# Performance work log

Measured on AMD Instinct MI355X. Metric: run time of the kernel, lower is better.

Reference implementation:

```python
import jax, jax.numpy as jnp
import numpy as np

N_NODES = 100000
N_EDGES = 1600000
IN_CH, HID, OUT_CH = 128, 64, 16
EPS = 1e-5


def _sage(x, src, dst, Ws, Wn, b):
    """DGL SAGEConv mean: fc_self(x) + fc_neigh(mean_{u in N(v)} x_u) + b."""
    msg = x[src]                                              # [E, F] gather
    agg = jax.ops.segment_sum(msg, dst, num_segments=N_NODES)  # [N, F]
    deg = jax.ops.segment_sum(jnp.ones((dst.shape[0],), x.dtype), dst,
                              num_segments=N_NODES)
    h_neigh = agg / jnp.maximum(deg, 1.0)[:, None]            # zero-deg -> 0
    return x @ Ws + h_neigh @ Wn + b


def _bn(h, gamma, beta):
    """BatchNorm1d, training-mode batch statistics (biased var)."""
    mean = jnp.mean(h, axis=0)
    var = jnp.mean(jnp.square(h - mean), axis=0)
    return (h - mean) * jax.lax.rsqrt(var + EPS) * gamma + beta


def setup_inputs() -> dict:
    key = jax.random.key(0)
    ks = jax.random.split(key, 20)
    s = 0.05
    d = {
        "x": jax.random.normal(ks[0], (N_NODES, IN_CH), jnp.float32),
        "src": jax.random.randint(ks[1], (N_EDGES,), 0, N_NODES),
        "dst": jax.random.randint(ks[2], (N_EDGES,), 0, N_NODES),
        # layer1: SAGEConv(128 -> 64) + BN
        "Ws1": jax.random.normal(ks[3], (IN_CH, HID), jnp.float32) * s,
        "Wn1": jax.random.normal(ks[4], (IN_CH, HID), jnp.float32) * s,
        "b1": jnp.zeros((HID,), jnp.float32),
        "g1": jnp.ones((HID,), jnp.float32),
        "be1": jnp.zeros((HID,), jnp.float32),
        # hidden layer A: SAGEConv(64 -> 64) + BN + ReLU
        "Ws2": jax.random.normal(ks[5], (HID, HID), jnp.float32) * s,
        "Wn2": jax.random.normal(ks[6], (HID, HID), jnp.float32) * s,
        "b2": jnp.zeros((HID,), jnp.float32),
        "g2": jnp.ones((HID,), jnp.float32),
        "be2": jnp.zeros((HID,), jnp.float32),
        # hidden layer B
        "Ws3": jax.random.normal(ks[7], (HID, HID), jnp.float32) * s,
        "Wn3": jax.random.normal(ks[8], (HID, HID), jnp.float32) * s,
        "b3": jnp.zeros((HID,), jnp.float32),
        "g3": jnp.ones((HID,), jnp.float32),
        "be3": jnp.zeros((HID,), jnp.float32),
        # output: SAGEConv(64 -> 16)
        "Ws4": jax.random.normal(ks[9], (HID, OUT_CH), jnp.float32) * s,
        "Wn4": jax.random.normal(ks[10], (HID, OUT_CH), jnp.float32) * s,
        "b4": jnp.zeros((OUT_CH,), jnp.float32),
    }
    return d


def reference(x, src, dst,
              Ws1, Wn1, b1, g1, be1,
              Ws2, Wn2, b2, g2, be2,
              Ws3, Wn3, b3, g3, be3,
              Ws4, Wn4, b4):
    h = _sage(x, src, dst, Ws1, Wn1, b1)
    h = _bn(h, g1, be1)                      # note: no ReLU after layer1 (as in source)
    h = jax.nn.relu(_bn(_sage(h, src, dst, Ws2, Wn2, b2), g2, be2))
    h = jax.nn.relu(_bn(_sage(h, src, dst, Ws3, Wn3, b3), g3, be3))
    h = _sage(h, src, dst, Ws4, Wn4, b4)
    return h
```

## Files before the change

kernel.cpp:

```cpp
#include <hip/hip_runtime.h>

#define BKT_SHIFT 9
#define BKT_SIZE 512


__device__ __forceinline__ float bfu(unsigned short h) {
    return __uint_as_float(((unsigned)h) << 16);
}
__device__ __forceinline__ unsigned short fbf(float f) {
    unsigned u = __float_as_uint(f);
    unsigned r = 0x7FFFu + ((u >> 16) & 1u);
    return (unsigned short)((u + r) >> 16);
}


__global__ __launch_bounds__(256) void fill_bf16(unsigned short* p, int n, float val) {
    int i = blockIdx.x * 256 + threadIdx.x;
    if (i < n) p[i] = fbf(val);
}

__global__ __launch_bounds__(256) void zero_i32(int* p, int n) {
    int i = blockIdx.x * 256 + threadIdx.x;
    if (i < n) p[i] = 0;
}

__global__ void detect_kernel(const unsigned* g1w, int* flags) {
    if (threadIdx.x == 0 && blockIdx.x == 0)
        flags[0] = (g1w[0] == 0x3F803F80u) ? 1 : 0;
}


__global__ __launch_bounds__(256)
void conv_all(const int* flags, float* wf,
              const void* a0, const void* a1, const void* a2, const void* a3,
              const void* a4, const void* a5, const void* a6, const void* a7,
              const void* a8, const void* a9, const void* a10, const void* a11,
              const void* a12, const void* a13, const void* a14, const void* a15,
              const void* a16, const void* a17) {
    const void* srcs[18] = {a0,a1,a2,a3,a4,a5,a6,a7,a8,a9,a10,a11,a12,a13,a14,a15,a16,a17};
    const int ns[18]   = {8192,8192,64,64,64,4096,4096,64,64,64,4096,4096,64,64,64,1024,1024,16};
    const int offs[18] = {0,8192,16384,16448,16512,16576,20672,24768,24832,24896,
                          24960,29056,33152,33216,33280,33344,34368,35392};
    int b = blockIdx.x;
    if (b >= 18) return;
    int n = ns[b];
    float* dst = wf + offs[b];
    int isbf = flags[0];
    if (isbf) {
        const unsigned short* s = (const unsigned short*)srcs[b];
        for (int i = threadIdx.x; i < n; i += 256) dst[i] = bfu(s[i]);
    } else {
        const float* s = (const float*)srcs[b];
        for (int i = threadIdx.x; i < n; i += 256) dst[i] = s[i];
    }
}


__global__ __launch_bounds__(256)
void bin_count(const int* dst, int* bcnt, int E, int NB, int CE) {
    __shared__ int hist[512];
    int t = threadIdx.x;
    for (int i = t; i < NB; i += 256) hist[i] = 0;
    __syncthreads();
    int beg = blockIdx.x * CE;
    int end = beg + CE; if (end > E) end = E;
    for (int i = beg + t; i < end; i += 256)
        atomicAdd(&hist[dst[i] >> BKT_SHIFT], 1);
    __syncthreads();
    for (int i = t; i < NB; i += 256)
        if (hist[i]) atomicAdd(&bcnt[i], hist[i]);
}

__global__ __launch_bounds__(256)
void bin_scan(const int* bcnt, int* boff, int* gcur, int NB, int E,
              int* rowptr, int Nn) {
    __shared__ int s2[256];
    int t = threadIdx.x;
    int i0 = 2 * t, i1 = 2 * t + 1;
    int c0 = (i0 < NB) ? bcnt[i0] : 0;
    int c1 = (i1 < NB) ? bcnt[i1] : 0;
    s2[t] = c0 + c1;
    __syncthreads();
    for (int off = 1; off < 256; off <<= 1) {
        int x = (t >= off) ? s2[t - off] : 0;
        __syncthreads();
        s2[t] += x;
        __syncthreads();
    }
    int excl = s2[t] - (c0 + c1);
    if (i0 < NB) { boff[i0] = excl;      gcur[i0] = excl; }
    if (i1 < NB) { boff[i1] = excl + c0; gcur[i1] = excl + c0; }
    if (t == 255) { boff[NB] = E; rowptr[Nn] = E; }
}

__global__ __launch_bounds__(256)
void bin_scatter(const int* src, const int* dst, int* gcur, unsigned* staging,
                 int E, int NB, int CE) {
    __shared__ int hist[512];
    __shared__ int cur[512];
    int t = threadIdx.x;
    for (int i = t; i < NB; i += 256) hist[i] = 0;
    __syncthreads();
    int beg = blockIdx.x * CE;
    int end = beg + CE; if (end > E) end = E;
    for (int i = beg + t; i < end; i += 256)
        atomicAdd(&hist[dst[i] >> BKT_SHIFT], 1);
    __syncthreads();
    for (int i = t; i < NB; i += 256) {
        int h = hist[i];
        cur[i] = h ? atomicAdd(&gcur[i], h) : 0;
    }
    __syncthreads();
    for (int i = beg + t; i < end; i += 256) {
        int d = dst[i];
        int b = d >> BKT_SHIFT;
        int pos = atomicAdd(&cur[b], 1);
        staging[pos] = ((unsigned)src[i] << BKT_SHIFT) | (unsigned)(d & (BKT_SIZE - 1));
    }
}

__global__ __launch_bounds__(256)
void bin_csr(const unsigned* staging, const int* boff, int* rowptr, int* esrc, int Nn) {
    __shared__ int sdeg[512];
    __shared__ int sscan[256];
    int b = blockIdx.x, t = threadIdx.x;
    int ebeg = boff[b], eend = boff[b + 1];
    int n0 = b << BKT_SHIFT;
    sdeg[t] = 0; sdeg[t + 256] = 0;
    __syncthreads();
    for (int i = ebeg + t; i < eend; i += 256)
        atomicAdd(&sdeg[staging[i] & (BKT_SIZE - 1)], 1);
    __syncthreads();
    int d0 = sdeg[2 * t], d1 = sdeg[2 * t + 1];
    sscan[t] = d0 + d1;
    __syncthreads();
    for (int off = 1; off < 256; off <<= 1) {
        int x = (t >= off) ? sscan[t - off] : 0;
        __syncthreads();
        sscan[t] += x;
        __syncthreads();
    }
    int excl = sscan[t] - (d0 + d1);
    int cur0 = ebeg + excl;
    int cur1 = cur0 + d0;
    int g0 = n0 + 2 * t, g1 = n0 + 2 * t + 1;
    if (g0 < Nn) rowptr[g0] = cur0;
    if (g1 < Nn) rowptr[g1] = cur1;
    __syncthreads();
    sdeg[2 * t] = cur0;
    sdeg[2 * t + 1] = cur1;
    __syncthreads();
    for (int i = ebeg + t; i < eend; i += 256) {
        unsigned pk = staging[i];
        int n = pk & (BKT_SIZE - 1);
        int pos = atomicAdd(&sdeg[n], 1);
        esrc[pos] = (int)(pk >> BKT_SHIFT);
    }
}


__global__ __launch_bounds__(256)
void gemm64(const void* Aptr, int K, const int* flags, int useflag,
            const float* Ws, const float* Wn,
            const float* bias, const float* aff, int affine, int relu,
            float* outS, unsigned short* outP, int Nn) {
    __shared__ float Wlds[16][128];
    __shared__ float Atile[16][128];

    const int tid = threadIdx.x;
    const int ty = tid >> 4;
    const int tx = tid & 15;
    const int r0 = blockIdx.x * 128;
    const int abf16 = useflag ? flags[0] : 0;

    float acc[8][8];
    for (int i = 0; i < 8; ++i)
        for (int j = 0; j < 8; ++j) acc[i][j] = 0.f;

    const int arow = tid >> 1;
    const int ahalf = (tid & 1) * 8;
    int aRowG = r0 + arow;
    if (aRowG >= Nn) aRowG = Nn - 1;

    const int wkl = tid >> 4;
    const int wjc = (tid & 15) * 8;

    const int nkc = K >> 4;
    for (int kc = 0; kc < nkc; ++kc) {
        const int k0 = kc << 4;
        __syncthreads();
        {
            const float* wsrc;
            if (wjc < 64) wsrc = Ws + (size_t)(k0 + wkl) * 64 + wjc;
            else          wsrc = Wn + (size_t)(k0 + wkl) * 64 + (wjc - 64);
            const float4* wp4 = reinterpret_cast<const float4*>(wsrc);
            float4 w0 = wp4[0], w1 = wp4[1];
            Wlds[wkl][wjc + 0] = w0.x; Wlds[wkl][wjc + 1] = w0.y;
            Wlds[wkl][wjc + 2] = w0.z; Wlds[wkl][wjc + 3] = w0.w;
            Wlds[wkl][wjc + 4] = w1.x; Wlds[wkl][wjc + 5] = w1.y;
            Wlds[wkl][wjc + 6] = w1.z; Wlds[wkl][wjc + 7] = w1.w;
        }
        {
            float v[8];
            if (abf16) {
                const unsigned short* Ab = (const unsigned short*)Aptr;
                uint4 u = *reinterpret_cast<const uint4*>(Ab + (size_t)aRowG * K + k0 + ahalf);
                v[0] = bfu((unsigned short)(u.x & 0xFFFF));
                v[1] = bfu((unsigned short)(u.x >> 16));
                v[2] = bfu((unsigned short)(u.y & 0xFFFF));
                v[3] = bfu((unsigned short)(u.y >> 16));
                v[4] = bfu((unsigned short)(u.z & 0xFFFF));
                v[5] = bfu((unsigned short)(u.z >> 16));
                v[6] = bfu((unsigned short)(u.w & 0xFFFF));
                v[7] = bfu((unsigned short)(u.w >> 16));
            } else {
                const float* Af = (const float*)Aptr;
                const float4* fp = reinterpret_cast<const float4*>(Af + (size_t)aRowG * K + k0 + ahalf);
                float4 f0 = fp[0], f1 = fp[1];
                v[0] = f0.x; v[1] = f0.y; v[2] = f0.z; v[3] = f0.w;
                v[4] = f1.x; v[5] = f1.y; v[6] = f1.z; v[7] = f1.w;
            }
            if (affine) {
                for (int j = 0; j < 8; ++j) {
                    int c = k0 + ahalf + j;
                    v[j] = v[j] * aff[c] + aff[K + c];
                    if (relu && v[j] < 0.f) v[j] = 0.f;
                }
            }
            for (int j = 0; j < 8; ++j) Atile[ahalf + j][arow] = v[j];
        }
        __syncthreads();
        for (int kk = 0; kk < 16; ++kk) {
            const float4* ap = reinterpret_cast<const float4*>(&Atile[kk][ty * 8]);
            float4 a0 = ap[0], a1 = ap[1];
            float a8[8];
            a8[0] = a0.x; a8[1] = a0.y; a8[2] = a0.z; a8[3] = a0.w;
            a8[4] = a1.x; a8[5] = a1.y; a8[6] = a1.z; a8[7] = a1.w;
            const float4* wp = reinterpret_cast<const float4*>(&Wlds[kk][tx * 8]);
            float4 w0 = wp[0], w1 = wp[1];
            float w8[8];
            w8[0] = w0.x; w8[1] = w0.y; w8[2] = w0.z; w8[3] = w0.w;
            w8[4] = w1.x; w8[5] = w1.y; w8[6] = w1.z; w8[7] = w1.w;
            for (int i = 0; i < 8; ++i)
                for (int j = 0; j < 8; ++j)
                    acc[i][j] = fmaf(a8[i], w8[j], acc[i][j]);
        }
    }
    const int cg = tx * 8;
    const int isS = (cg < 64) ? 1 : 0;
    const int cb = isS ? cg : (cg - 64);
    float badd[8];
    for (int j = 0; j < 8; ++j) badd[j] = isS ? bias[cb + j] : 0.f;
    for (int i = 0; i < 8; ++i) {
        int gr = r0 + ty * 8 + i;
        if (gr < Nn) {
            float res[8];
            for (int j = 0; j < 8; ++j) res[j] = acc[i][j] + badd[j];
            if (isS) {
                float* dp = outS + (size_t)gr * 64 + cb;
                float4 o0, o1;
                o0.x = res[0]; o0.y = res[1]; o0.z = res[2]; o0.w = res[3];
                o1.x = res[4]; o1.y = res[5]; o1.z = res[6]; o1.w = res[7];
                *reinterpret_cast<float4*>(dp) = o0;
                *reinterpret_cast<float4*>(dp + 4) = o1;
            } else {
                uint4 o;
                o.x = ((unsigned)fbf(res[1]) << 16) | (unsigned)fbf(res[0]);
                o.y = ((unsigned)fbf(res[3]) << 16) | (unsigned)fbf(res[2]);
                o.z = ((unsigned)fbf(res[5]) << 16) | (unsigned)fbf(res[4]);
                o.w = ((unsigned)fbf(res[7]) << 16) | (unsigned)fbf(res[6]);
                *reinterpret_cast<uint4*>(outP + (size_t)gr * 64 + cb) = o;
            }
        }
    }
}


__global__ __launch_bounds__(256)
void gemm16(const float* Aptr, const float* Ws, const float* Wn,
            const float* bias, const float* aff,
            float* outS, float* outP, int Nn) {
    __shared__ float Wlds[16][32];
    __shared__ float Atile[16][128];

    const int tid = threadIdx.x;
    const int ty = tid >> 4;
    const int tx = tid & 15;
    const int r0 = blockIdx.x * 128;
    const int K = 64;

    float acc[8][2];
    for (int i = 0; i < 8; ++i) { acc[i][0] = 0.f; acc[i][1] = 0.f; }

    const int arow = tid >> 1;
    const int ahalf = (tid & 1) * 8;
    int aRowG = r0 + arow;
    if (aRowG >= Nn) aRowG = Nn - 1;

    const int wkl = tid >> 4;
    const int wjc = (tid & 15) * 2;

    for (int kc = 0; kc < 4; ++kc) {
        const int k0 = kc << 4;
        __syncthreads();
        {
            const float* wsrc;
            if (wjc < 16) wsrc = Ws + (size_t)(k0 + wkl) * 16 + wjc;
            else          wsrc = Wn + (size_t)(k0 + wkl) * 16 + (wjc - 16);
            const float2* w2 = reinterpret_cast<const float2*>(wsrc);
            float2 w = w2[0];
            Wlds[wkl][wjc + 0] = w.x;
            Wlds[wkl][wjc + 1] = w.y;
        }
        {
            const float4* fp = reinterpret_cast<const float4*>(Aptr + (size_t)aRowG * K + k0 + ahalf);
            float4 f0 = fp[0], f1 = fp[1];
            float v[8];
            v[0] = f0.x; v[1] = f0.y; v[2] = f0.z; v[3] = f0.w;
            v[4] = f1.x; v[5] = f1.y; v[6] = f1.z; v[7] = f1.w;
            for (int j = 0; j < 8; ++j) {
                int c = k0 + ahalf + j;
                float t = v[j] * aff[c] + aff[K + c];
                if (t < 0.f) t = 0.f;
                Atile[ahalf + j][arow] = t;
            }
        }
        __syncthreads();
        for (int kk = 0; kk < 16; ++kk) {
            const float4* ap = reinterpret_cast<const float4*>(&Atile[kk][ty * 8]);
            float4 a0 = ap[0], a1 = ap[1];
            float a8[8];
            a8[0] = a0.x; a8[1] = a0.y; a8[2] = a0.z; a8[3] = a0.w;
            a8[4] = a1.x; a8[5] = a1.y; a8[6] = a1.z; a8[7] = a1.w;
            const float2* wp2 = reinterpret_cast<const float2*>(&Wlds[kk][tx * 2]);
            float2 w = wp2[0];
            for (int i = 0; i < 8; ++i) {
                acc[i][0] = fmaf(a8[i], w.x, acc[i][0]);
                acc[i][1] = fmaf(a8[i], w.y, acc[i][1]);
            }
        }
    }
    const int cg = tx * 2;
    const int isS = (cg < 16) ? 1 : 0;
    float* outp = isS ? outS : outP;
    const int cb = isS ? cg : (cg - 16);
    float b0 = isS ? bias[cb] : 0.f;
    float b1 = isS ? bias[cb + 1] : 0.f;
    for (int i = 0; i < 8; ++i) {
        int gr = r0 + ty * 8 + i;
        if (gr < Nn) {
            float2 o;
            o.x = acc[i][0] + b0;
            o.y = acc[i][1] + b1;
            *reinterpret_cast<float2*>(outp + (size_t)gr * 16 + cb) = o;
        }
    }
}


__global__ __launch_bounds__(256)
void agg64(const unsigned short* p, const float* s, const int* rowptr, const int* esrc,
           float* out, int Nn) {
    int v = (blockIdx.x << 2) + (threadIdx.x >> 6);
    if (v >= Nn) return;
    int lane = threadIdx.x & 63;
    int g = lane >> 4;
    int q = lane & 15;
    int beg = rowptr[v], end = rowptr[v + 1];
    float a0 = 0.f, a1 = 0.f, a2 = 0.f, a3 = 0.f;
    int e = beg + g;
    for (; e + 4 < end; e += 8) {
        int u0 = esrc[e];
        int u1 = esrc[e + 4];
        uint2 x0 = *reinterpret_cast<const uint2*>(p + (size_t)u0 * 64 + q * 4);
        uint2 x1 = *reinterpret_cast<const uint2*>(p + (size_t)u1 * 64 + q * 4);
        a0 += bfu((unsigned short)(x0.x & 0xFFFF)) + bfu((unsigned short)(x1.x & 0xFFFF));
        a1 += bfu((unsigned short)(x0.x >> 16))    + bfu((unsigned short)(x1.x >> 16));
        a2 += bfu((unsigned short)(x0.y & 0xFFFF)) + bfu((unsigned short)(x1.y & 0xFFFF));
        a3 += bfu((unsigned short)(x0.y >> 16))    + bfu((unsigned short)(x1.y >> 16));
    }
    for (; e < end; e += 4) {
        int u = esrc[e];
        uint2 x = *reinterpret_cast<const uint2*>(p + (size_t)u * 64 + q * 4);
        a0 += bfu((unsigned short)(x.x & 0xFFFF));
        a1 += bfu((unsigned short)(x.x >> 16));
        a2 += bfu((unsigned short)(x.y & 0xFFFF));
        a3 += bfu((unsigned short)(x.y >> 16));
    }
    a0 += __shfl_xor(a0, 16, 64); a0 += __shfl_xor(a0, 32, 64);
    a1 += __shfl_xor(a1, 16, 64); a1 += __shfl_xor(a1, 32, 64);
    a2 += __shfl_xor(a2, 16, 64); a2 += __shfl_xor(a2, 32, 64);
    a3 += __shfl_xor(a3, 16, 64); a3 += __shfl_xor(a3, 32, 64);
    if (g == 0) {
        float dd = (float)(end - beg);
        if (dd < 1.f) dd = 1.f;
        float inv = 1.f / dd;
        size_t o = (size_t)v * 64 + q * 4;
        float4 r;
        r.x = s[o + 0] + a0 * inv;
        r.y = s[o + 1] + a1 * inv;
        r.z = s[o + 2] + a2 * inv;
        r.w = s[o + 3] + a3 * inv;
        *reinterpret_cast<float4*>(out + o) = r;
    }
}


__global__ __launch_bounds__(256)
void agg16(const float* p, const float* s, const int* rowptr, const int* esrc,
           void* outv, const int* flags, int Nn) {
    int v = (blockIdx.x << 2) + (threadIdx.x >> 6);
    if (v >= Nn) return;
    int lane = threadIdx.x & 63;
    int g = lane >> 4;
    int c = lane & 15;
    int beg = rowptr[v], end = rowptr[v + 1];
    float a = 0.f;
    int e = beg + g;
    for (; e + 4 < end; e += 8) {
        int u0 = esrc[e];
        int u1 = esrc[e + 4];
        a += p[(size_t)u0 * 16 + c] + p[(size_t)u1 * 16 + c];
    }
    for (; e < end; e += 4) a += p[(size_t)esrc[e] * 16 + c];
    a += __shfl_xor(a, 16, 64);
    a += __shfl_xor(a, 32, 64);
    if (g == 0) {
        float dd = (float)(end - beg);
        if (dd < 1.f) dd = 1.f;
        float res = s[(size_t)v * 16 + c] + a / dd;
        if (flags[0]) ((unsigned short*)outv)[(size_t)v * 16 + c] = fbf(res);
        else          ((float*)outv)[(size_t)v * 16 + c] = res;
    }
}


__global__ __launch_bounds__(256) void stats_kernel(const float* h, float* stats, int Nn) {
    __shared__ float sh[512];
    int c = threadIdx.x & 63, g = threadIdx.x >> 6;
    float sm = 0.f, s2 = 0.f;
    for (int r = blockIdx.x * 4 + g; r < Nn; r += gridDim.x * 4) {
        float v = h[(size_t)r * 64 + c];
        sm += v; s2 += v * v;
    }
    sh[threadIdx.x] = sm;
    sh[256 + threadIdx.x] = s2;
    __syncthreads();
    if (g == 0) {
        float ts = sh[c] + sh[64 + c] + sh[128 + c] + sh[192 + c];
        float t2 = sh[256 + c] + sh[320 + c] + sh[384 + c] + sh[448 + c];
        atomicAdd(&stats[c], ts);
        atomicAdd(&stats[64 + c], t2);
    }
}

__global__ void affine_kernel(const float* stats, const float* g,
                              const float* be, float* aff, int Nn) {
    int c = threadIdx.x;
    if (c < 64) {
        float inv = 1.f / (float)Nn;
        float mean = stats[c] * inv;
        float var = stats[64 + c] * inv - mean * mean;
        float rstd = rsqrtf(var + 1e-5f);
        float sc = rstd * g[c];
        aff[c] = sc;
        aff[64 + c] = be[c] - mean * sc;
    }
}


extern "C" void kernel_launch(void* const* d_in, const int* in_sizes, int n_in,
                              void* d_out, int out_size, void* d_ws, size_t ws_size,
                              hipStream_t stream) {
    const void* x = d_in[0];
    const int* src = (const int*)d_in[1];
    const int* dst = (const int*)d_in[2];

    unsigned short* out_bf = (unsigned short*)d_out;
    const int ob = (out_size + 255) / 256;

    const int Nn = out_size / 16;
    const int E = in_sizes[1];

    if (Nn <= 0 || in_sizes[0] != Nn * 128 || in_sizes[2] != E || E <= 0 || n_in < 21
        || Nn > 256 * 1024) {
        fill_bf16<<<ob, 256, 0, stream>>>(out_bf, out_size, 21.0f);
        return;
    }

    size_t off = 0;
    char* base = (char*)d_ws;
    int* rowptr;     { rowptr  = (int*)(base + off); off += ((size_t)(Nn + 1) * 4 + 255) & ~(size_t)255; }
    int* esrc;       { esrc    = (int*)(base + off); off += ((size_t)E * 4 + 255) & ~(size_t)255; }
    unsigned* staging; { staging = (unsigned*)(base + off); off += ((size_t)E * 4 + 255) & ~(size_t)255; }
    unsigned short* bufP; { bufP = (unsigned short*)(base + off); off += ((size_t)Nn * 64 * 2 + 255) & ~(size_t)255; }
    float* bufS;     { bufS    = (float*)(base + off); off += ((size_t)Nn * 64 * 4 + 255) & ~(size_t)255; }
    float* stats;    { stats   = (float*)(base + off); off += 512; }
    float* aff;      { aff     = (float*)(base + off); off += 512; }
    int* flags;      { flags   = (int*)(base + off); off += 256; }
    int* bcnt;       { bcnt    = (int*)(base + off); off += 2048; }
    int* boff;       { boff    = (int*)(base + off); off += 2304; }
    int* gcur;       { gcur    = (int*)(base + off); off += 2048; }
    float* wf;       { wf      = (float*)(base + off); off += ((size_t)35408 * 4 + 255) & ~(size_t)255; }
    float* s4 = (float*)bufP;
    float* p4 = s4 + (size_t)Nn * 16;

    if (off > ws_size) {
        fill_bf16<<<ob, 256, 0, stream>>>(out_bf, out_size, 13.0f);
        return;
    }

    const float* WS1 = wf + 0;      const float* WN1 = wf + 8192;
    const float* B1  = wf + 16384;  const float* G1  = wf + 16448;  const float* BE1 = wf + 16512;
    const float* WS2 = wf + 16576;  const float* WN2 = wf + 20672;
    const float* B2  = wf + 24768;  const float* G2  = wf + 24832;  const float* BE2 = wf + 24896;
    const float* WS3 = wf + 24960;  const float* WN3 = wf + 29056;
    const float* B3  = wf + 33152;  const float* G3  = wf + 33216;  const float* BE3 = wf + 33280;
    const float* WS4 = wf + 33344;  const float* WN4 = wf + 34368;
    const float* B4  = wf + 35392;

    detect_kernel<<<1, 64, 0, stream>>>((const unsigned*)d_in[6], flags);
    conv_all<<<18, 256, 0, stream>>>(flags, wf,
        d_in[3], d_in[4], d_in[5], d_in[6], d_in[7],
        d_in[8], d_in[9], d_in[10], d_in[11], d_in[12],
        d_in[13], d_in[14], d_in[15], d_in[16], d_in[17],
        d_in[18], d_in[19], d_in[20]);

    const int NB = (Nn + BKT_SIZE - 1) >> BKT_SHIFT;
    const int NBC = 192;
    const int CE = (E + NBC - 1) / NBC;
    zero_i32<<<2, 256, 0, stream>>>(bcnt, NB);
    bin_count<<<NBC, 256, 0, stream>>>(dst, bcnt, E, NB, CE);
    bin_scan<<<1, 256, 0, stream>>>(bcnt, boff, gcur, NB, E, rowptr, Nn);
    bin_scatter<<<NBC, 256, 0, stream>>>(src, dst, gcur, staging, E, NB, CE);
    bin_csr<<<NB, 256, 0, stream>>>(staging, boff, rowptr, esrc, Nn);

    const int gb = (Nn + 127) / 128;
    const int ab = (Nn + 3) / 4;

    gemm64<<<gb, 256, 0, stream>>>(x, 128, flags, 1, WS1, WN1, B1, aff, 0, 0, bufS, bufP, Nn);
    agg64<<<ab, 256, 0, stream>>>(bufP, bufS, rowptr, esrc, bufS, Nn);
    zero_i32<<<1, 256, 0, stream>>>((int*)stats, 128);
    stats_kernel<<<240, 256, 0, stream>>>(bufS, stats, Nn);
    affine_kernel<<<1, 64, 0, stream>>>(stats, G1, BE1, aff, Nn);

    gemm64<<<gb, 256, 0, stream>>>(bufS, 64, flags, 0, WS2, WN2, B2, aff, 1, 0, bufS, bufP, Nn);
    agg64<<<ab, 256, 0, stream>>>(bufP, bufS, rowptr, esrc, bufS, Nn);
    zero_i32<<<1, 256, 0, stream>>>((int*)stats, 128);
    stats_kernel<<<240, 256, 0, stream>>>(bufS, stats, Nn);
    affine_kernel<<<1, 64, 0, stream>>>(stats, G2, BE2, aff, Nn);

    gemm64<<<gb, 256, 0, stream>>>(bufS, 64, flags, 0, WS3, WN3, B3, aff, 1, 1, bufS, bufP, Nn);
    agg64<<<ab, 256, 0, stream>>>(bufP, bufS, rowptr, esrc, bufS, Nn);
    zero_i32<<<1, 256, 0, stream>>>((int*)stats, 128);
    stats_kernel<<<240, 256, 0, stream>>>(bufS, stats, Nn);
    affine_kernel<<<1, 64, 0, stream>>>(stats, G3, BE3, aff, Nn);

    gemm16<<<gb, 256, 0, stream>>>(bufS, WS4, WN4, B4, aff, s4, p4, Nn);
    agg16<<<ab, 256, 0, stream>>>(p4, s4, rowptr, esrc, d_out, flags, Nn);
}
```

Measured before the change: 606.9 us.

## Replace FP32 SIMT GEMM with bf16 MFMA kernel using prepacked weights

Replaces the scalar-FMA 128x128-tile GEMM for the three 64-wide layers with a 64-row-tile kernel built on the 16x16x32 bf16 MFMA instruction. A new pack_w kernel converts the weights into the MFMA B-fragment layout. Activations are converted to bf16 in LDS, and the self-projection output is now stored as bf16 in a buffer aliased with the edge staging area, which cuts its write and read traffic. The cost is lower precision for the self term and the inputs, three extra small launches, and scalar 2-byte output stores.

After: 564.4 us. -7.0%, faster.

```diff
diff --git a/kernel.cpp b/kernel.cpp
--- a/kernel.cpp
+++ b/kernel.cpp
@@ -2,6 +2,9 @@
 
 #define BKT_SHIFT 9
 #define BKT_SIZE 512
+
+typedef __attribute__((ext_vector_type(8))) short short8;
+typedef __attribute__((ext_vector_type(4))) float floatx4;
 
 
 __device__ __forceinline__ float bfu(unsigned short h) {
@@ -57,6 +60,26 @@
 
 
 __global__ __launch_bounds__(256)
+void pack_w(const float* Ws, const float* Wn, unsigned short* out, int K) {
+    int tid = blockIdx.x * 256 + threadIdx.x;
+    int total = (K >> 5) * 8 * 64;
+    if (tid >= total) return;
+    int l = tid & 63;
+    int tn = (tid >> 6) & 7;
+    int kc = tid >> 9;
+    int col = tn * 16 + (l & 15);
+    int kb = kc * 32 + (l >> 4) * 8;
+    unsigned short v[8];
+    for (int j = 0; j < 8; ++j) {
+        int k = kb + j;
+        float f = (col < 64) ? Ws[(size_t)k * 64 + col] : Wn[(size_t)k * 64 + (col - 64)];
+        v[j] = fbf(f);
+    }
+    *reinterpret_cast<uint4*>(out + (size_t)tid * 8) = *reinterpret_cast<uint4*>(v);
+}
+
+
+__global__ __launch_bounds__(256)
 void bin_count(const int* dst, int* bcnt, int E, int NB, int CE) {
     __shared__ int hist[512];
     int t = threadIdx.x;
@@ -160,116 +183,79 @@
 
 
 __global__ __launch_bounds__(256)
-void gemm64(const void* Aptr, int K, const int* flags, int useflag,
-            const float* Ws, const float* Wn,
-            const float* bias, const float* aff, int affine, int relu,
-            float* outS, unsigned short* outP, int Nn) {
-    __shared__ float Wlds[16][128];
-    __shared__ float Atile[16][128];
+void gemm64m(const void* Aptr, int K, const int* flags, int useflag,
+             const unsigned short* Wpk, const float* bias, const float* aff,
+             int affine, int relu,
+             unsigned short* outS, unsigned short* outP, int Nn) {
+    __shared__ unsigned short Ald[64 * 40];
 
     const int tid = threadIdx.x;
-    const int ty = tid >> 4;
-    const int tx = tid & 15;
-    const int r0 = blockIdx.x * 128;
+    const int wave = tid >> 6;
+    const int lane = tid & 63;
+    const int lrow = lane & 15;
+    const int lq = lane >> 4;
+    const int r0 = blockIdx.x * 64;
+    const int wrow = wave * 16;
     const int abf16 = useflag ? flags[0] : 0;
 
-    float acc[8][8];
-    for (int i = 0; i < 8; ++i)
-        for (int j = 0; j < 8; ++j) acc[i][j] = 0.f;
-
-    const int arow = tid >> 1;
-    const int ahalf = (tid & 1) * 8;
+    floatx4 acc[8];
+    for (int t = 0; t < 8; ++t)
+        for (int i = 0; i < 4; ++i) acc[t][i] = 0.f;
+
+    const int arow = tid >> 2;
+    const int akq = tid & 3;
     int aRowG = r0 + arow;
     if (aRowG >= Nn) aRowG = Nn - 1;
 
-    const int wkl = tid >> 4;
-    const int wjc = (tid & 15) * 8;
-
-    const int nkc = K >> 4;
+    const int nkc = K >> 5;
     for (int kc = 0; kc < nkc; ++kc) {
-        const int k0 = kc << 4;
-        __syncthreads();
-        {
-            const float* wsrc;
-            if (wjc < 64) wsrc = Ws + (size_t)(k0 + wkl) * 64 + wjc;
-            else          wsrc = Wn + (size_t)(k0 + wkl) * 64 + (wjc - 64);
-            const float4* wp4 = reinterpret_cast<const float4*>(wsrc);
-            float4 w0 = wp4[0], w1 = wp4[1];
-            Wlds[wkl][wjc + 0] = w0.x; Wlds[wkl][wjc + 1] = w0.y;
-            Wlds[wkl][wjc + 2] = w0.z; Wlds[wkl][wjc + 3] = w0.w;
-            Wlds[wkl][wjc + 4] = w1.x; Wlds[wkl][wjc + 5] = w1.y;
-            Wlds[wkl][wjc + 6] = w1.z; Wlds[wkl][wjc + 7] = w1.w;
-        }
-        {
+        const int k0 = kc << 5;
+        __syncthreads();
+        if (abf16) {
+            const unsigned short* Ab = (const unsigned short*)Aptr;
+            uint4 u = *reinterpret_cast<const uint4*>(Ab + (size_t)aRowG * K + k0 + akq * 8);
+            *reinterpret_cast<uint4*>(&Ald[arow * 40 + akq * 8]) = u;
+        } else {
+            const float* Af = (const float*)Aptr;
+            const float4* fp = reinterpret_cast<const float4*>(Af + (size_t)aRowG * K + k0 + akq * 8);
+            float4 f0 = fp[0], f1 = fp[1];
             float v[8];
-            if (abf16) {
-                const unsigned short* Ab = (const unsigned short*)Aptr;
-                uint4 u = *reinterpret_cast<const uint4*>(Ab + (size_t)aRowG * K + k0 + ahalf);
-                v[0] = bfu((unsigned short)(u.x & 0xFFFF));
-                v[1] = bfu((unsigned short)(u.x >> 16));
-                v[2] = bfu((unsigned short)(u.y & 0xFFFF));
-                v[3] = bfu((unsigned short)(u.y >> 16));
-                v[4] = bfu((unsigned short)(u.z & 0xFFFF));
-                v[5] = bfu((unsigned short)(u.z >> 16));
-                v[6] = bfu((unsigned short)(u.w & 0xFFFF));
-                v[7] = bfu((unsigned short)(u.w >> 16));
-            } else {
-                const float* Af = (const float*)Aptr;
-                const float4* fp = reinterpret_cast<const float4*>(Af + (size_t)aRowG * K + k0 + ahalf);
-                float4 f0 = fp[0], f1 = fp[1];
-                v[0] = f0.x; v[1] = f0.y; v[2] = f0.z; v[3] = f0.w;
-                v[4] = f1.x; v[5] = f1.y; v[6] = f1.z; v[7] = f1.w;
-            }
+            v[0] = f0.x; v[1] = f0.y; v[2] = f0.z; v[3] = f0.w;
+            v[4] = f1.x; v[5] = f1.y; v[6] = f1.z; v[7] = f1.w;
             if (affine) {
                 for (int j = 0; j < 8; ++j) {
-                    int c = k0 + ahalf + j;
+                    int c = k0 + akq * 8 + j;
                     v[j] = v[j] * aff[c] + aff[K + c];
                     if (relu && v[j] < 0.f) v[j] = 0.f;
                 }
             }
-            for (int j = 0; j < 8; ++j) Atile[ahalf + j][arow] = v[j];
-        }
-        __syncthreads();
-        for (int kk = 0; kk < 16; ++kk) {
-            const float4* ap = reinterpret_cast<const float4*>(&Atile[kk][ty * 8]);
-            float4 a0 = ap[0], a1 = ap[1];
-            float a8[8];
-            a8[0] = a0.x; a8[1] = a0.y; a8[2] = a0.z; a8[3] = a0.w;
-            a8[4] = a1.x; a8[5] = a1.y; a8[6] = a1.z; a8[7] = a1.w;
-            const float4* wp = reinterpret_cast<const float4*>(&Wlds[kk][tx * 8]);
-            float4 w0 = wp[0], w1 = wp[1];
-            float w8[8];
-            w8[0] = w0.x; w8[1] = w0.y; w8[2] = w0.z; w8[3] = w0.w;
-            w8[4] = w1.x; w8[5] = w1.y; w8[6] = w1.z; w8[7] = w1.w;
-            for (int i = 0; i < 8; ++i)
-                for (int j = 0; j < 8; ++j)
-                    acc[i][j] = fmaf(a8[i], w8[j], acc[i][j]);
-        }
-    }
-    const int cg = tx * 8;
-    const int isS = (cg < 64) ? 1 : 0;
-    const int cb = isS ? cg : (cg - 64);
-    float badd[8];
-    for (int j = 0; j < 8; ++j) badd[j] = isS ? bias[cb + j] : 0.f;
-    for (int i = 0; i < 8; ++i) {
-        int gr = r0 + ty * 8 + i;
-        if (gr < Nn) {
-            float res[8];
-            for (int j = 0; j < 8; ++j) res[j] = acc[i][j] + badd[j];
-            if (isS) {
-                float* dp = outS + (size_t)gr * 64 + cb;
-                float4 o0, o1;
-                o0.x = res[0]; o0.y = res[1]; o0.z = res[2]; o0.w = res[3];
-                o1.x = res[4]; o1.y = res[5]; o1.z = res[6]; o1.w = res[7];
-                *reinterpret_cast<float4*>(dp) = o0;
-                *reinterpret_cast<float4*>(dp + 4) = o1;
-            } else {
-                uint4 o;
-                o.x = ((unsigned)fbf(res[1]) << 16) | (unsigned)fbf(res[0]);
-                o.y = ((unsigned)fbf(res[3]) << 16) | (unsigned)fbf(res[2]);
-                o.z = ((unsigned)fbf(res[5]) << 16) | (unsigned)fbf(res[4]);
-                o.w = ((unsigned)fbf(res[7]) << 16) | (unsigned)fbf(res[6]);
-                *reinterpret_cast<uint4*>(outP + (size_t)gr * 64 + cb) = o;
+            uint4 u;
+            u.x = ((unsigned)fbf(v[1]) << 16) | (unsigned)fbf(v[0]);
+            u.y = ((unsigned)fbf(v[3]) << 16) | (unsigned)fbf(v[2]);
+            u.z = ((unsigned)fbf(v[5]) << 16) | (unsigned)fbf(v[4]);
+            u.w = ((unsigned)fbf(v[7]) << 16) | (unsigned)fbf(v[6]);
+            *reinterpret_cast<uint4*>(&Ald[arow * 40 + akq * 8]) = u;
+        }
+        __syncthreads();
+        short8 afr = *reinterpret_cast<const short8*>(&Ald[(wrow + lrow) * 40 + lq * 8]);
+        const short8* bp = reinterpret_cast<const short8*>(Wpk) + ((size_t)kc * 8) * 64 + lane;
+#pragma unroll
+        for (int tn = 0; tn < 8; ++tn) {
+            short8 bfr = bp[tn * 64];
+            acc[tn] = __builtin_amdgcn_mfma_f32_16x16x32_bf16(afr, bfr, acc[tn], 0, 0, 0);
+        }
+    }
+#pragma unroll
+    for (int tn = 0; tn < 8; ++tn) {
+        int col = tn * 16 + lrow;
+        float badd = (tn < 4) ? bias[col] : 0.f;
+#pragma unroll
+        for (int r = 0; r < 4; ++r) {
+            int gr = r0 + wrow + lq * 4 + r;
+            if (gr < Nn) {
+                float v = acc[tn][r] + badd;
+                if (tn < 4) outS[(size_t)gr * 64 + col] = fbf(v);
+                else        outP[(size_t)gr * 64 + (col - 64)] = fbf(v);
             }
         }
     }
@@ -359,8 +345,8 @@
 
 
 __global__ __launch_bounds__(256)
-void agg64(const unsigned short* p, const float* s, const int* rowptr, const int* esrc,
-           float* out, int Nn) {
+void agg64(const unsigned short* p, const unsigned short* s, const int* rowptr,
+           const int* esrc, float* out, int Nn) {
     int v = (blockIdx.x << 2) + (threadIdx.x >> 6);
     if (v >= Nn) return;
     int lane = threadIdx.x & 63;
@@ -396,11 +382,12 @@
         if (dd < 1.f) dd = 1.f;
         float inv = 1.f / dd;
         size_t o = (size_t)v * 64 + q * 4;
+        uint2 su = *reinterpret_cast<const uint2*>(s + o);
         float4 r;
-        r.x = s[o + 0] + a0 * inv;
-        r.y = s[o + 1] + a1 * inv;
-        r.z = s[o + 2] + a2 * inv;
-        r.w = s[o + 3] + a3 * inv;
+        r.x = bfu((unsigned short)(su.x & 0xFFFF)) + a0 * inv;
+        r.y = bfu((unsigned short)(su.x >> 16))    + a1 * inv;
+        r.z = bfu((unsigned short)(su.y & 0xFFFF)) + a2 * inv;
+        r.w = bfu((unsigned short)(su.y >> 16))    + a3 * inv;
         *reinterpret_cast<float4*>(out + o) = r;
     }
 }
@@ -490,18 +477,26 @@
 
     size_t off = 0;
     char* base = (char*)d_ws;
-    int* rowptr;     { rowptr  = (int*)(base + off); off += ((size_t)(Nn + 1) * 4 + 255) & ~(size_t)255; }
-    int* esrc;       { esrc    = (int*)(base + off); off += ((size_t)E * 4 + 255) & ~(size_t)255; }
-    unsigned* staging; { staging = (unsigned*)(base + off); off += ((size_t)E * 4 + 255) & ~(size_t)255; }
+    int* rowptr;  { rowptr = (int*)(base + off); off += ((size_t)(Nn + 1) * 4 + 255) & ~(size_t)255; }
+    int* esrc;    { esrc   = (int*)(base + off); off += ((size_t)E * 4 + 255) & ~(size_t)255; }
+    unsigned* staging; unsigned short* sbuf;
+    {
+        size_t sz1 = (size_t)E * 4, sz2 = (size_t)Nn * 64 * 2;
+        size_t sz = sz1 > sz2 ? sz1 : sz2;
+        staging = (unsigned*)(base + off);
+        sbuf = (unsigned short*)(base + off);
+        off += (sz + 255) & ~(size_t)255;
+    }
     unsigned short* bufP; { bufP = (unsigned short*)(base + off); off += ((size_t)Nn * 64 * 2 + 255) & ~(size_t)255; }
-    float* bufS;     { bufS    = (float*)(base + off); off += ((size_t)Nn * 64 * 4 + 255) & ~(size_t)255; }
-    float* stats;    { stats   = (float*)(base + off); off += 512; }
-    float* aff;      { aff     = (float*)(base + off); off += 512; }
-    int* flags;      { flags   = (int*)(base + off); off += 256; }
-    int* bcnt;       { bcnt    = (int*)(base + off); off += 2048; }
-    int* boff;       { boff    = (int*)(base + off); off += 2304; }
-    int* gcur;       { gcur    = (int*)(base + off); off += 2048; }
-    float* wf;       { wf      = (float*)(base + off); off += ((size_t)35408 * 4 + 255) & ~(size_t)255; }
+    float* bufS;  { bufS  = (float*)(base + off); off += ((size_t)Nn * 64 * 4 + 255) & ~(size_t)255; }
+    float* stats; { stats = (float*)(base + off); off += 512; }
+    float* aff;   { aff   = (float*)(base + off); off += 512; }
+    int* flags;   { flags = (int*)(base + off); off += 256; }
+    int* bcnt;    { bcnt  = (int*)(base + off); off += 2048; }
+    int* boff;    { boff  = (int*)(base + off); off += 2304; }
+    int* gcur;    { gcur  = (int*)(base + off); off += 2048; }
+    float* wf;    { wf    = (float*)(base + off); off += ((size_t)35408 * 4 + 255) & ~(size_t)255; }
+    unsigned short* wpk; { wpk = (unsigned short*)(base + off); off += ((size_t)32768 * 2 + 255) & ~(size_t)255; }
     float* s4 = (float*)bufP;
     float* p4 = s4 + (size_t)Nn * 16;
 
@@ -518,6 +513,9 @@
     const float* B3  = wf + 33152;  const float* G3  = wf + 33216;  const float* BE3 = wf + 33280;
     const float* WS4 = wf + 33344;  const float* WN4 = wf + 34368;
     const float* B4  = wf + 35392;
+    unsigned short* WPK1 = wpk + 0;
+    unsigned short* WPK2 = wpk + 16384;
+    unsigned short* WPK3 = wpk + 24576;
 
     detect_kernel<<<1, 64, 0, stream>>>((const unsigned*)d_in[6], flags);
     conv_all<<<18, 256, 0, stream>>>(flags, wf,
@@ -525,6 +523,9 @@
         d_in[8], d_in[9], d_in[10], d_in[11], d_in[12],
         d_in[13], d_in[14], d_in[15], d_in[16], d_in[17],
         d_in[18], d_in[19], d_in[20]);
+    pack_w<<<8, 256, 0, stream>>>(WS1, WN1, WPK1, 128);
+    pack_w<<<4, 256, 0, stream>>>(WS2, WN2, WPK2, 64);
+    pack_w<<<4, 256, 0, stream>>>(WS3, WN3, WPK3, 64);
 
     const int NB = (Nn + BKT_SIZE - 1) >> BKT_SHIFT;
     const int NBC = 192;
@@ -535,23 +536,24 @@
     bin_scatter<<<NBC, 256, 0, stream>>>(src, dst, gcur, staging, E, NB, CE);
     bin_csr<<<NB, 256, 0, stream>>>(staging, boff, rowptr, esrc, Nn);
 
+    const int gmb = (Nn + 63) / 64;
+    const int ab = (Nn + 3) / 4;
     const int gb = (Nn + 127) / 128;
-    const int ab = (Nn + 3) / 4;
-
-    gemm64<<<gb, 256, 0, stream>>>(x, 128, flags, 1, WS1, WN1, B1, aff, 0, 0, bufS, bufP, Nn);
-    agg64<<<ab, 256, 0, stream>>>(bufP, bufS, rowptr, esrc, bufS, Nn);
+
+    gemm64m<<<gmb, 256, 0, stream>>>(x, 128, flags, 1, WPK1, B1, aff, 0, 0, sbuf, bufP, Nn);
+    agg64<<<ab, 256, 0, stream>>>(bufP, sbuf, rowptr, esrc, bufS, Nn);
     zero_i32<<<1, 256, 0, stream>>>((int*)stats, 128);
     stats_kernel<<<240, 256, 0, stream>>>(bufS, stats, Nn);
     affine_kernel<<<1, 64, 0, stream>>>(stats, G1, BE1, aff, Nn);
 
-    gemm64<<<gb, 256, 0, stream>>>(bufS, 64, flags, 0, WS2, WN2, B2, aff, 1, 0, bufS, bufP, Nn);
-    agg64<<<ab, 256, 0, stream>>>(bufP, bufS, rowptr, esrc, bufS, Nn);
+    gemm64m<<<gmb, 256, 0, stream>>>(bufS, 64, flags, 0, WPK2, B2, aff, 1, 0, sbuf, bufP, Nn);
+    agg64<<<ab, 256, 0, stream>>>(bufP, sbuf, rowptr, esrc, bufS, Nn);
     zero_i32<<<1, 256, 0, stream>>>((int*)stats, 128);
     stats_kernel<<<240, 256, 0, stream>>>(bufS, stats, Nn);
     affine_kernel<<<1, 64, 0, stream>>>(stats, G2, BE2, aff, Nn);
 
-    gemm64<<<gb, 256, 0, stream>>>(bufS, 64, flags, 0, WS3, WN3, B3, aff, 1, 1, bufS, bufP, Nn);
-    agg64<<<ab, 256, 0, stream>>>(bufP, bufS, rowptr, esrc, bufS, Nn);
+    gemm64m<<<gmb, 256, 0, stream>>>(bufS, 64, flags, 0, WPK3, B3, aff, 1, 1, sbuf, bufP, Nn);
+    agg64<<<ab, 256, 0, stream>>>(bufP, sbuf, rowptr, esrc, bufS, Nn);
     zero_i32<<<1, 256, 0, stream>>>((int*)stats, 128);
     stats_kernel<<<240, 256, 0, stream>>>(bufS, stats, Nn);
     affine_kernel<<<1, 64, 0, stream>>>(stats, G3, BE3, aff, Nn);
```
